# Kernel tuning notes

Hardware: AMD Instinct MI355X
Metric: run time of the kernel (lower is better)

Reference implementation:

```python
import jax, jax.numpy as jnp
import numpy as np

GAMMA = 1.0
BIG = 1e30  # finite stand-in for +inf (safe under logsumexp and autodiff)


def setup_inputs() -> dict:
    key = jax.random.key(0)
    kx, ky = jax.random.split(key)
    x = jax.random.normal(kx, (32, 512, 64), dtype=jnp.float32)
    y = jax.random.normal(ky, (32, 512, 64), dtype=jnp.float32)
    return {"x": x, "y": y}


def _cosine_dist(x, y):
    # 1 - cosine similarity; matches F.normalize(p=2, eps=1e-12)
    xn = x / jnp.maximum(jnp.linalg.norm(x, axis=-1, keepdims=True), 1e-12)
    yn = y / jnp.maximum(jnp.linalg.norm(y, axis=-1, keepdims=True), 1e-12)
    return 1.0 - jnp.einsum('btd,bsd->bts', xn, yn)


def _soft_dtw(D, gamma):
    # Anti-diagonal soft-DTW DP. D: [B, T1, T2] -> [B]
    B, T1, T2 = D.shape
    R0 = jnp.full((B, T1 + 1, T2 + 1), BIG, dtype=D.dtype).at[:, 0, 0].set(0.0)
    i = jnp.arange(1, T1 + 1)  # all rows; each diagonal k has j = k - i

    def step(R, k):
        j = k - i
        valid = (j >= 1) & (j <= T2)
        jc = jnp.where(valid, j, 0)  # clamp invalid lanes; masked below
        cost = jnp.where(valid, D[:, i - 1, jnp.clip(jc - 1, 0, T2 - 1)], 0.0)
        r_diag = R[:, i - 1, jnp.clip(jc - 1, 0, T2)]
        r_left = R[:, i, jnp.clip(jc - 1, 0, T2)]
        r_up = R[:, i - 1, jc]
        stacked = jnp.stack([r_diag, r_left, r_up], axis=0)  # [3, B, T1]
        stacked = jnp.where(valid[None, None, :], stacked, 0.0)
        soft_min = -gamma * jax.nn.logsumexp(-stacked / gamma, axis=0)
        new = cost + soft_min
        old = R[:, i, jc]
        R = R.at[:, i, jc].set(jnp.where(valid[None, :], new, old))
        return R, None

    ks = jnp.arange(2, T1 + T2 + 1)
    R, _ = jax.lax.scan(step, R0, ks)
    return R[:, T1, T2]


def reference(x, y):
    D_xy = _cosine_dist(x, y)
    D_xx = _cosine_dist(x, x)
    D_yy = _cosine_dist(y, y)
    sdtw_xy = _soft_dtw(D_xy, GAMMA)
    sdtw_xx = _soft_dtw(D_xx, GAMMA)
    sdtw_yy = _soft_dtw(D_yy, GAMMA)
    return sdtw_xy - 0.5 * (sdtw_xx + sdtw_yy)
```

## Files before the change

kernel.cpp:

```cpp
#include <hip/hip_runtime.h>
#include <hip/hip_fp16.h>

#define T1 512
#define NB 32
#define NP 96
#define DHEAD 64

#define RSLOTS 128
#define RBYTES (RSLOTS * 1024)
#define PFD 32

typedef __attribute__((ext_vector_type(8))) short bf16x8;
typedef __attribute__((ext_vector_type(4))) float f32x4;
typedef __attribute__((ext_vector_type(4))) unsigned int u32x4;

__global__ __launch_bounds__(256) void k_normalize(const float* __restrict__ x,
                                                   const float* __restrict__ y,
                                                   ushort* __restrict__ xb,
                                                   ushort* __restrict__ yb) {
  int wid  = threadIdx.x >> 6;
  int lane = threadIdx.x & 63;
  int row  = blockIdx.x * 4 + wid;
  const float* src; ushort* dst;
  if (row < NB * T1) { src = x + (size_t)row * DHEAD;            dst = xb + (size_t)row * DHEAD; }
  else { int r2 = row - NB * T1; src = y + (size_t)r2 * DHEAD;   dst = yb + (size_t)r2 * DHEAD; }
  float v = src[lane];
  float s = v * v;
  #pragma unroll
  for (int off = 32; off > 0; off >>= 1) s += __shfl_xor(s, off);
  float rn = 1.0f / fmaxf(sqrtf(s), 1e-12f);
  float o = v * rn;
  unsigned u = __float_as_uint(o);
  unsigned r = (u + 0x7fffu + ((u >> 16) & 1u)) >> 16;
  dst[lane] = (ushort)r;
}

__global__ __launch_bounds__(256) void k_gemm_w(const ushort* __restrict__ xb,
                                                const ushort* __restrict__ yb,
                                                __half* __restrict__ W) {
  int pb = blockIdx.z;
  int p  = pb >> 5;
  int b  = pb & 31;
  const ushort* A  = ((p == 2) ? yb : xb) + (size_t)b * T1 * DHEAD;
  const ushort* Bm = ((p == 1) ? xb : yb) + (size_t)b * T1 * DHEAD;

  int wid = threadIdx.x >> 6, lane = threadIdx.x & 63;
  int wm = wid >> 1, wn = wid & 1;
  int i0 = blockIdx.x * 128 + wm * 64;
  int j0 = blockIdx.y * 128 + wn * 64;
  int lr = lane & 15, kg = lane >> 4;

  f32x4 acc[4][4];
  #pragma unroll
  for (int ic = 0; ic < 4; ++ic)
    #pragma unroll
    for (int jc = 0; jc < 4; ++jc) acc[ic][jc] = (f32x4){0.f, 0.f, 0.f, 0.f};

  #pragma unroll
  for (int kk = 0; kk < 2; ++kk) {
    int ko = kk * 32 + kg * 8;
    bf16x8 af[4], bf[4];
    #pragma unroll
    for (int ic = 0; ic < 4; ++ic)
      af[ic] = *reinterpret_cast<const bf16x8*>(A + (size_t)(i0 + ic * 16 + lr) * DHEAD + ko);
    #pragma unroll
    for (int jc = 0; jc < 4; ++jc)
      bf[jc] = *reinterpret_cast<const bf16x8*>(Bm + (size_t)(j0 + jc * 16 + lr) * DHEAD + ko);
    #pragma unroll
    for (int ic = 0; ic < 4; ++ic)
      #pragma unroll
      for (int jc = 0; jc < 4; ++jc)
        acc[ic][jc] = __builtin_amdgcn_mfma_f32_16x16x32_bf16(af[ic], bf[jc], acc[ic][jc], 0, 0, 0);
  }

  const float NLOG2E = -1.44269504088896340736f;
  __half* Wp = W + (size_t)pb * (T1 * T1);
  int ib = kg << 2;
  #pragma unroll
  for (int ic = 0; ic < 4; ++ic) {
    int i = i0 + ic * 16 + ib;
    #pragma unroll
    for (int jc = 0; jc < 4; ++jc) {
      int j = j0 + jc * 16 + lr;
      union { __half h[4]; uint2 u; } pk;
      #pragma unroll
      for (int r = 0; r < 4; ++r) {
        float d = 1.0f - acc[ic][jc][r];
        pk.h[r] = __float2half(exp2f(NLOG2E * d));
      }
      *reinterpret_cast<uint2*>(Wp + (size_t)j * T1 + i) = pk.u;
    }
  }
}

__global__ __launch_bounds__(64, 1) void k_dtw(const __half* __restrict__ W,
                                               float* __restrict__ res) {
  __shared__ __attribute__((aligned(16))) char ring[RBYTES];
  const int prob = blockIdx.x;
  const __half* Wp = W + (size_t)prob * (T1 * T1);
  const int lane = threadIdx.x;

  float Va[8], Vb[8];
  #pragma unroll
  for (int r = 0; r < 8; ++r) { Va[r] = 0.f; Vb[r] = 0.f; }
  float B2 = 0.f, B2p = 0.f;
  const float dgSeed = (lane == 0) ? 1.0f : 0.0f;

  auto dppshr = [](float v) -> float {
    return __int_as_float(__builtin_amdgcn_update_dpp(
        0, __float_as_int(v), 0x138 , 0xF, 0xF, true));
  };

  const char* gsrc = (const char*)Wp + (size_t)PFD * 1024 + (lane << 4);
  unsigned lslot = (PFD << 10) & (RBYTES - 1);

  #pragma unroll
  for (int c = 0; c < PFD; ++c) {
    const __half* gp = Wp + ((size_t)c << 9) + (lane << 3);
    __builtin_amdgcn_global_load_lds(
        (const __attribute__((address_space(1))) void*)gp,
        (__attribute__((address_space(3))) void*)(ring + ((unsigned)(c << 10))), 16, 0, 0);
  }
  asm volatile("s_waitcnt vmcnt(24)" ::: "memory");

  u32x4 d0, d1, d2, d3, d4, d5, d6, d7;
  unsigned va0, va1, va2, va3, va4, va5, va6, va7;
#define RS_INIT(K) do { \
    d##K = *reinterpret_cast<const u32x4*>( \
        ring + ((((unsigned)(K - lane) & 127u) << 10) | (unsigned)(lane << 4))); \
    va##K = ((((unsigned)(8 + K - lane) & 127u) << 10) | (unsigned)(lane << 4)); \
  } while (0)
  RS_INIT(0); RS_INIT(1); RS_INIT(2); RS_INIT(3);
  RS_INIT(4); RS_INIT(5); RS_INIT(6); RS_INIT(7);
#undef RS_INIT

#define DTW_STEP(KK, VIN, VOUT, SDG, SEEDK, GUARD) do {                       \
    const int t_ = tb + (KK);                                                 \
    float nbUp_ = dppshr(VIN[7]);                    \
    float nbDg_ = dppshr(VOUT[7]);                   \
    float up_ = nbUp_ * sUp;                                                  \
    float dg_ = nbDg_ * (SDG);                                                \
    if (SEEDK) dg_ = dgSeed;                                                  \
    union { u32x4 u; __half h[8]; } cv_; cv_.u = d##KK;                       \
    d##KK = *reinterpret_cast<const u32x4*>(ring + va##KK);     \
    va##KK = (va##KK + 8192u) & (RBYTES - 1);                                 \
    __builtin_amdgcn_global_load_lds(                          \
        (const __attribute__((address_space(1))) void*)gsrc,                  \
        (__attribute__((address_space(3))) void*)(ring + lslot), 16, 0, 0);   \
    lslot = (lslot + 1024u) & (RBYTES - 1);                                   \
    gsrc += ((t_ + PFD) < T1 - 1) ? 1024 : 0;           \
    float wv_[8];                                                             \
    _Pragma("unroll")                                                         \
    for (int r = 0; r < 8; ++r) wv_[r] = __half2float(cv_.h[r]);              \
    bool act_ = true;                                                         \
    if (GUARD) { int j_ = t_ - lane; act_ = ((unsigned)j_ < (unsigned)T1); }  \
    if (act_) {                                                               \
      float c_ = fmaf(wv_[0], up_, wv_[0] * (dg_ + VIN[0]));                  \
      VOUT[0] = c_;                                                           \
      _Pragma("unroll")                                                       \
      for (int r = 1; r < 8; ++r) {                                           \
        c_ = fmaf(wv_[r], c_, wv_[r] * (VIN[r-1] + VIN[r]));                  \
        VOUT[r] = c_;                                                         \
      }                                                                       \
      if ((KK) == 7) {                                 \
        float m_ = fmaxf(fmaxf(fmaxf(VOUT[0],VOUT[1]),fmaxf(VOUT[2],VOUT[3])),\
                         fmaxf(fmaxf(VOUT[4],VOUT[5]),fmaxf(VOUT[6],VOUT[7])));\
        int e_ = (int)((__float_as_uint(m_) >> 23) & 0xFF) - 127;             \
        e_ = e_ < -126 ? -126 : (e_ > 126 ? 126 : e_);                        \
        float sc_ = __uint_as_float((unsigned)(127 - e_) << 23);              \
        _Pragma("unroll")                                                     \
        for (int r = 0; r < 8; ++r) VOUT[r] *= sc_;                           \
        B2p = B2; B2 -= (float)e_;                                            \
      }                                                                       \
    }                                                                         \
  } while (0)

#define DTW_GROUP(GUARD, SEED) do {                                           \
    asm volatile("s_waitcnt vmcnt(16)" ::: "memory");      \
    float nbBn_ = dppshr(B2);                 \
    float nbBo_ = dppshr(B2p);                \
    float sUp  = __uint_as_float(                                             \
        (unsigned)(127 + (int)fminf(fmaxf(B2 - nbBn_, -120.f), 120.f)) << 23);\
    float sDg0 = __uint_as_float(                                             \
        (unsigned)(127 + (int)fminf(fmaxf(B2 - nbBo_, -120.f), 120.f)) << 23);\
    DTW_STEP(0, Va, Vb, sDg0, SEED, GUARD);                                   \
    DTW_STEP(1, Vb, Va, sUp, false, GUARD);                                   \
    DTW_STEP(2, Va, Vb, sUp, false, GUARD);                                   \
    DTW_STEP(3, Vb, Va, sUp, false, GUARD);                                   \
    DTW_STEP(4, Va, Vb, sUp, false, GUARD);                                   \
    DTW_STEP(5, Vb, Va, sUp, false, GUARD);                                   \
    DTW_STEP(6, Va, Vb, sUp, false, GUARD);                                   \
    DTW_STEP(7, Vb, Va, sUp, false, GUARD);                                   \
  } while (0)

  { const int tb = 0; DTW_GROUP(true, true); }
  #pragma unroll 1
  for (int tb = 8; tb < 64; tb += 8)  DTW_GROUP(true, false);
  #pragma unroll 1
  for (int tb = 64; tb < 568; tb += 8) DTW_GROUP(false, false);
  { const int tb = 568; DTW_GROUP(true, false); }

  if (lane == 63) {
    res[prob] = (B2 - log2f(Va[7])) * 0.69314718055994530942f;
  }
#undef DTW_STEP
#undef DTW_GROUP
}

__global__ void k_combine(const float* __restrict__ res, float* __restrict__ out) {
  int b = threadIdx.x;
  if (b < NB) out[b] = res[b] - 0.5f * (res[NB + b] + res[2 * NB + b]);
}

extern "C" void kernel_launch(void* const* d_in, const int* in_sizes, int n_in,
                              void* d_out, int out_size, void* d_ws, size_t ws_size,
                              hipStream_t stream) {
  const float* x = (const float*)d_in[0];
  const float* y = (const float*)d_in[1];
  float* out = (float*)d_out;

  const size_t xb_off  = 0;
  const size_t yb_off  = (size_t)NB * T1 * DHEAD * sizeof(ushort);
  const size_t W_off   = 2 * yb_off;
  const size_t res_off = W_off + (size_t)3 * NB * T1 * T1 * sizeof(__half);
  const size_t need    = res_off + NP * sizeof(float);

  if (ws_size < need) {
    hipMemsetAsync(d_out, 0xFF, (size_t)out_size * sizeof(float), stream);
    return;
  }

  ushort* xb  = (ushort*)((char*)d_ws + xb_off);
  ushort* yb  = (ushort*)((char*)d_ws + yb_off);
  __half* W   = (__half*)((char*)d_ws + W_off);
  float*  res = (float*)((char*)d_ws + res_off);

  hipLaunchKernelGGL(k_normalize, dim3(8192), dim3(256), 0, stream, x, y, xb, yb);
  hipLaunchKernelGGL(k_gemm_w, dim3(4, 4, 96), dim3(256), 0, stream, xb, yb, W);
  hipLaunchKernelGGL(k_dtw, dim3(NP), dim3(64), 0, stream, W, res);
  hipLaunchKernelGGL(k_combine, dim3(1), dim3(64), 0, stream, res, out);
}
```

Baseline: 92.18 us.

## Split soft-DTW rows across two wavefronts with LDS handoff and pipelined start

```diff
diff --git a/kernel.cpp b/kernel.cpp
--- a/kernel.cpp
+++ b/kernel.cpp
@@ -7,12 +7,12 @@
 #define DHEAD 64
 
 #define RSLOTS 128
-#define RBYTES (RSLOTS * 1024)
-#define PFD 32
+#define WRING  65536
+#define PFD 24
+#define NIDLE 9
 
 typedef __attribute__((ext_vector_type(8))) short bf16x8;
 typedef __attribute__((ext_vector_type(4))) float f32x4;
-typedef __attribute__((ext_vector_type(4))) unsigned int u32x4;
 
 __global__ __launch_bounds__(256) void k_normalize(const float* __restrict__ x,
                                                    const float* __restrict__ y,
@@ -93,118 +93,179 @@
   }
 }
 
-__global__ __launch_bounds__(64, 1) void k_dtw(const __half* __restrict__ W,
-                                               float* __restrict__ res) {
-  __shared__ __attribute__((aligned(16))) char ring[RBYTES];
+__global__ __launch_bounds__(128, 1) void k_dtw(const __half* __restrict__ W,
+                                                float* __restrict__ res) {
+  __shared__ __attribute__((aligned(16))) char ring[2 * WRING];
+  __shared__ __attribute__((aligned(16))) float hval[RSLOTS];
+  __shared__ float hbase[32];
   const int prob = blockIdx.x;
   const __half* Wp = W + (size_t)prob * (T1 * T1);
-  const int lane = threadIdx.x;
-
-  float Va[8], Vb[8];
-  #pragma unroll
-  for (int r = 0; r < 8; ++r) { Va[r] = 0.f; Vb[r] = 0.f; }
+  const int tid  = threadIdx.x;
+  const int lane = tid & 63;
+  const int w    = __builtin_amdgcn_readfirstlane(tid >> 6);
+
+  const char* gbase = (const char*)Wp + (w << 9);
+  char* ringw = ring + (w << 16);
+
+  float Va[4], Vb[4];
+  #pragma unroll
+  for (int r = 0; r < 4; ++r) { Va[r] = 0.f; Vb[r] = 0.f; }
   float B2 = 0.f, B2p = 0.f;
-  const float dgSeed = (lane == 0) ? 1.0f : 0.0f;
+  float cSave = 0.f;
+  float dgl0  = 0.f;
+  unsigned hw = 256;
 
   auto dppshr = [](float v) -> float {
     return __int_as_float(__builtin_amdgcn_update_dpp(
         0, __float_as_int(v), 0x138 , 0xF, 0xF, true));
   };
 
-  const char* gsrc = (const char*)Wp + (size_t)PFD * 1024 + (lane << 4);
-  unsigned lslot = (PFD << 10) & (RBYTES - 1);
+#define SCALEBITS(dexp) __uint_as_float( \
+    (unsigned)(127 + (int)fminf(fmaxf((dexp), -120.f), 120.f)) << 23)
+
+#define GLL4(GP, LP) __builtin_amdgcn_global_load_lds( \
+    (const __attribute__((address_space(1))) void*)(GP), \
+    (__attribute__((address_space(3))) void*)(LP), 4, 0, 0)
 
   #pragma unroll
   for (int c = 0; c < PFD; ++c) {
-    const __half* gp = Wp + ((size_t)c << 9) + (lane << 3);
-    __builtin_amdgcn_global_load_lds(
-        (const __attribute__((address_space(1))) void*)gp,
-        (__attribute__((address_space(3))) void*)(ring + ((unsigned)(c << 10))), 16, 0, 0);
-  }
-  asm volatile("s_waitcnt vmcnt(24)" ::: "memory");
-
-  u32x4 d0, d1, d2, d3, d4, d5, d6, d7;
+    const char* gp = gbase + ((size_t)c << 10);
+    char* lp = ringw + ((unsigned)c << 9);
+    GLL4(gp + (lane << 2), lp);
+    GLL4(gp + 256 + (lane << 2), lp + 256);
+  }
+  asm volatile("s_waitcnt vmcnt(32)" ::: "memory");
+
+  uint2 d0, d1, d2, d3, d4, d5, d6, d7;
   unsigned va0, va1, va2, va3, va4, va5, va6, va7;
 #define RS_INIT(K) do { \
-    d##K = *reinterpret_cast<const u32x4*>( \
-        ring + ((((unsigned)(K - lane) & 127u) << 10) | (unsigned)(lane << 4))); \
-    va##K = ((((unsigned)(8 + K - lane) & 127u) << 10) | (unsigned)(lane << 4)); \
+    d##K = *reinterpret_cast<const uint2*>( \
+        ringw + ((((unsigned)((K) - lane) & 127u) << 9) | (unsigned)(lane << 3))); \
+    va##K = ((((unsigned)((K) + 8 - lane) & 127u) << 9) | (unsigned)(lane << 3)); \
   } while (0)
-  RS_INIT(0); RS_INIT(1); RS_INIT(2); RS_INIT(3);
-  RS_INIT(4); RS_INIT(5); RS_INIT(6); RS_INIT(7);
+  RS_INIT(0); RS_INIT(1); RS_INIT(2); RS_INIT(3); RS_INIT(4); RS_INIT(5); RS_INIT(6);
 #undef RS_INIT
-
-#define DTW_STEP(KK, VIN, VOUT, SDG, SEEDK, GUARD) do {                       \
+  va7 = ((((unsigned)(7 - lane) & 127u) << 9) | (unsigned)(lane << 3));
+
+#define DTW_STEP2(KK, VIN, VOUT, SDG, SEEDK, GUARD, ISW0) do {                \
     const int t_ = tb + (KK);                                                 \
-    float nbUp_ = dppshr(VIN[7]);                    \
-    float nbDg_ = dppshr(VOUT[7]);                   \
+    if (ISW0) {                        \
+      if (lane == 63) {                                                       \
+        *reinterpret_cast<float*>(reinterpret_cast<char*>(hval) + hw) = cSave;\
+        if ((KK) == 0) hbase[(tb >> 3) & 31] = B2;                            \
+      }                                                                       \
+      hw = (hw + 4u) & 511u;                                                  \
+    }                                                                         \
+    float nbUp_ = dppshr(VIN[3]);                    \
+    float nbDg_ = dppshr(VOUT[3]);                   \
     float up_ = nbUp_ * sUp;                                                  \
     float dg_ = nbDg_ * (SDG);                                                \
-    if (SEEDK) dg_ = dgSeed;                                                  \
-    union { u32x4 u; __half h[8]; } cv_; cv_.u = d##KK;                       \
-    d##KK = *reinterpret_cast<const u32x4*>(ring + va##KK);     \
-    va##KK = (va##KK + 8192u) & (RBYTES - 1);                                 \
-    __builtin_amdgcn_global_load_lds(                          \
-        (const __attribute__((address_space(1))) void*)gsrc,                  \
-        (__attribute__((address_space(3))) void*)(ring + lslot), 16, 0, 0);   \
-    lslot = (lslot + 1024u) & (RBYTES - 1);                                   \
-    gsrc += ((t_ + PFD) < T1 - 1) ? 1024 : 0;           \
-    float wv_[8];                                                             \
-    _Pragma("unroll")                                                         \
-    for (int r = 0; r < 8; ++r) wv_[r] = __half2float(cv_.h[r]);              \
+    if (!ISW0) {                               \
+      float hup_ = hv[KK] * ((KK) == 0 ? sH0 : sH1);                          \
+      up_ = (lane == 0) ? hup_ : up_;                                         \
+      dg_ = (lane == 0) ? dgl0 : dg_;                                         \
+      dgl0 = hup_;                                                            \
+    }                                                                         \
+    if (SEEDK) dg_ = (lane == 0) ? 1.0f : dg_;          \
+    union { uint2 u; __half h[4]; } cv_; cv_.u = d##KK;                       \
+    if ((KK) != 7) {                               \
+      d##KK = *reinterpret_cast<const uint2*>(ringw + va##KK);                \
+      va##KK = (va##KK + 4096u) & (WRING - 1);                                \
+    }                                                                         \
+    { int cc_ = t_ + PFD; cc_ = cc_ > T1 - 1 ? T1 - 1 : cc_;                  \
+      const char* gp_ = gbase + ((size_t)cc_ << 10);                          \
+      char* lp_ = ringw + (((unsigned)cc_ & 127u) << 9);                      \
+      GLL4(gp_ + (lane << 2), lp_);                                           \
+      GLL4(gp_ + 256 + (lane << 2), lp_ + 256);                               \
+    }                                                                         \
+    float w0_ = __half2float(cv_.h[0]), w1_ = __half2float(cv_.h[1]);         \
+    float w2_ = __half2float(cv_.h[2]), w3_ = __half2float(cv_.h[3]);         \
     bool act_ = true;                                                         \
     if (GUARD) { int j_ = t_ - lane; act_ = ((unsigned)j_ < (unsigned)T1); }  \
     if (act_) {                                                               \
-      float c_ = fmaf(wv_[0], up_, wv_[0] * (dg_ + VIN[0]));                  \
-      VOUT[0] = c_;                                                           \
-      _Pragma("unroll")                                                       \
-      for (int r = 1; r < 8; ++r) {                                           \
-        c_ = fmaf(wv_[r], c_, wv_[r] * (VIN[r-1] + VIN[r]));                  \
-        VOUT[r] = c_;                                                         \
-      }                                                                       \
+      float c_ = fmaf(w0_, up_, w0_ * (dg_ + VIN[0]));  VOUT[0] = c_;         \
+      c_ = fmaf(w1_, c_, w1_ * (VIN[0] + VIN[1]));      VOUT[1] = c_;         \
+      c_ = fmaf(w2_, c_, w2_ * (VIN[1] + VIN[2]));      VOUT[2] = c_;         \
+      c_ = fmaf(w3_, c_, w3_ * (VIN[2] + VIN[3]));      VOUT[3] = c_;         \
+      if (ISW0) cSave = c_;                     \
       if ((KK) == 7) {                                 \
-        float m_ = fmaxf(fmaxf(fmaxf(VOUT[0],VOUT[1]),fmaxf(VOUT[2],VOUT[3])),\
-                         fmaxf(fmaxf(VOUT[4],VOUT[5]),fmaxf(VOUT[6],VOUT[7])));\
+        float m_ = fmaxf(fmaxf(VOUT[0], VOUT[1]), fmaxf(VOUT[2], VOUT[3]));   \
         int e_ = (int)((__float_as_uint(m_) >> 23) & 0xFF) - 127;             \
         e_ = e_ < -126 ? -126 : (e_ > 126 ? 126 : e_);                        \
         float sc_ = __uint_as_float((unsigned)(127 - e_) << 23);              \
-        _Pragma("unroll")                                                     \
-        for (int r = 0; r < 8; ++r) VOUT[r] *= sc_;                           \
+        VOUT[0] *= sc_; VOUT[1] *= sc_; VOUT[2] *= sc_; VOUT[3] *= sc_;       \
+        if (!ISW0) dgl0 *= sc_;                                               \
         B2p = B2; B2 -= (float)e_;                                            \
       }                                                                       \
     }                                                                         \
   } while (0)
 
-#define DTW_GROUP(GUARD, SEED) do {                                           \
+#define DTW_GROUP2(GUARD, SEED, ISW0) do {                                    \
+    if (ISW0) { asm volatile("s_waitcnt lgkmcnt(0)" ::: "memory"); }          \
+    __builtin_amdgcn_s_barrier();                                             \
+    asm volatile("" ::: "memory");                                            \
     asm volatile("s_waitcnt vmcnt(16)" ::: "memory");      \
-    float nbBn_ = dppshr(B2);                 \
-    float nbBo_ = dppshr(B2p);                \
-    float sUp  = __uint_as_float(                                             \
-        (unsigned)(127 + (int)fminf(fmaxf(B2 - nbBn_, -120.f), 120.f)) << 23);\
-    float sDg0 = __uint_as_float(                                             \
-        (unsigned)(127 + (int)fminf(fmaxf(B2 - nbBo_, -120.f), 120.f)) << 23);\
-    DTW_STEP(0, Va, Vb, sDg0, SEED, GUARD);                                   \
-    DTW_STEP(1, Vb, Va, sUp, false, GUARD);                                   \
-    DTW_STEP(2, Va, Vb, sUp, false, GUARD);                                   \
-    DTW_STEP(3, Vb, Va, sUp, false, GUARD);                                   \
-    DTW_STEP(4, Va, Vb, sUp, false, GUARD);                                   \
-    DTW_STEP(5, Vb, Va, sUp, false, GUARD);                                   \
-    DTW_STEP(6, Va, Vb, sUp, false, GUARD);                                   \
-    DTW_STEP(7, Vb, Va, sUp, false, GUARD);                                   \
+    d7 = *reinterpret_cast<const uint2*>(ringw + va7);     \
+    va7 = (va7 + 4096u) & (WRING - 1);                                        \
+    float nbBn_ = dppshr(B2);                                                 \
+    float nbBo_ = dppshr(B2p);                                                \
+    float sUp  = SCALEBITS(B2 - nbBn_);                                       \
+    float sDg0 = SCALEBITS(B2 - nbBo_);                                       \
+    float hv[8] = {0.f,0.f,0.f,0.f,0.f,0.f,0.f,0.f};                          \
+    float sH0 = 0.f, sH1 = 0.f;                                               \
+    if (!ISW0) {                                                              \
+      int c0_ = tb & 127;                                  \
+      f32x4 ha_ = *reinterpret_cast<const f32x4*>(hval + c0_);                \
+      f32x4 hb_ = *reinterpret_cast<const f32x4*>(hval + c0_ + 4);            \
+      hv[0]=ha_[0]; hv[1]=ha_[1]; hv[2]=ha_[2]; hv[3]=ha_[3];                 \
+      hv[4]=hb_[0]; hv[5]=hb_[1]; hv[6]=hb_[2]; hv[7]=hb_[3];                 \
+      int wg_ = (tb >> 3) + 8;                                                \
+      sH1 = SCALEBITS(B2 - hbase[wg_ & 31]);               \
+      sH0 = SCALEBITS(B2 - hbase[(wg_ - 1) & 31]);  \
+    }                                                                         \
+    DTW_STEP2(0, Va, Vb, sDg0, SEED,  GUARD, ISW0);                           \
+    DTW_STEP2(1, Vb, Va, sUp,  false, GUARD, ISW0);                           \
+    DTW_STEP2(2, Va, Vb, sUp,  false, GUARD, ISW0);                           \
+    DTW_STEP2(3, Vb, Va, sUp,  false, GUARD, ISW0);                           \
+    DTW_STEP2(4, Va, Vb, sUp,  false, GUARD, ISW0);                           \
+    DTW_STEP2(5, Vb, Va, sUp,  false, GUARD, ISW0);                           \
+    DTW_STEP2(6, Va, Vb, sUp,  false, GUARD, ISW0);                           \
+    DTW_STEP2(7, Vb, Va, sUp,  false, GUARD, ISW0);                           \
   } while (0)
 
-  { const int tb = 0; DTW_GROUP(true, true); }
-  #pragma unroll 1
-  for (int tb = 8; tb < 64; tb += 8)  DTW_GROUP(true, false);
-  #pragma unroll 1
-  for (int tb = 64; tb < 568; tb += 8) DTW_GROUP(false, false);
-  { const int tb = 568; DTW_GROUP(true, false); }
-
-  if (lane == 63) {
-    res[prob] = (B2 - log2f(Va[7])) * 0.69314718055994530942f;
-  }
-#undef DTW_STEP
-#undef DTW_GROUP
+  if (w == 0) {
+    { const int tb = 0; DTW_GROUP2(true, true, 1); }
+    #pragma unroll 1
+    for (int tb = 8; tb < 64; tb += 8)   DTW_GROUP2(true,  false, 1);
+    #pragma unroll 1
+    for (int tb = 64; tb < 568; tb += 8) DTW_GROUP2(false, false, 1);
+    { const int tb = 568; DTW_GROUP2(true, false, 1); }
+    #pragma unroll 1
+    for (int i = 0; i < NIDLE; ++i) {
+      asm volatile("s_waitcnt lgkmcnt(0)" ::: "memory");
+      __builtin_amdgcn_s_barrier();
+      asm volatile("" ::: "memory");
+    }
+  } else {
+    #pragma unroll 1
+    for (int i = 0; i < NIDLE; ++i) {
+      __builtin_amdgcn_s_barrier();
+      asm volatile("" ::: "memory");
+    }
+    #pragma unroll 1
+    for (int tb = 0; tb < 64; tb += 8)   DTW_GROUP2(true,  false, 0);
+    #pragma unroll 1
+    for (int tb = 64; tb < 568; tb += 8) DTW_GROUP2(false, false, 0);
+    { const int tb = 568; DTW_GROUP2(true, false, 0); }
+  }
+
+  if (w == 1 && lane == 63) {
+    res[prob] = (B2 - log2f(Vb[3])) * 0.69314718055994530942f;
+  }
+#undef DTW_STEP2
+#undef DTW_GROUP2
+#undef SCALEBITS
+#undef GLL4
 }
 
 __global__ void k_combine(const float* __restrict__ res, float* __restrict__ out) {
@@ -237,6 +298,6 @@
 
   hipLaunchKernelGGL(k_normalize, dim3(8192), dim3(256), 0, stream, x, y, xb, yb);
   hipLaunchKernelGGL(k_gemm_w, dim3(4, 4, 96), dim3(256), 0, stream, xb, yb, W);
-  hipLaunchKernelGGL(k_dtw, dim3(NP), dim3(64), 0, stream, W, res);
+  hipLaunchKernelGGL(k_dtw, dim3(NP), dim3(128), 0, stream, W, res);
   hipLaunchKernelGGL(k_combine, dim3(1), dim3(64), 0, stream, res, out);
 }
```

Result: slower. 197.0 us (+113.7%).
